# Performance work log

Measured on AMD Instinct MI355X. Metric: run time of the kernel, lower is better.

The kernel has to match this reference:

```python
import jax, jax.numpy as jnp
import numpy as np

M = 16            # num_frequencies
DIM = 512         # dim_input
B = 32768         # flattened batch
H = M + 1         # raw complex table side
N = 2 * M + 1     # autocorrelated table side
NPAR = H * H      # (m+1)^2


def setup_inputs() -> dict:
    key = jax.random.key(0)
    k1, k2, k3 = jax.random.split(key, 3)
    inputs = jax.random.normal(k1, (B, DIM), dtype=jnp.float32)
    targets = jax.random.uniform(k2, (B, 2), dtype=jnp.float32)  # points in [0,1) subset of [-1,1]^2
    # nn.init.normal_(weight, 0.01) => mean=0.01, std=1.0 ; bias zeros
    W = jax.random.normal(k3, (2 * NPAR, DIM), dtype=jnp.float32) + 0.01
    b = jnp.zeros((2 * NPAR,), dtype=jnp.float32)
    return {"inputs": inputs, "targets": targets, "W": W, "b": b}


def reference(inputs, targets, W, b):
    # Linear -> unconstrained complex (m+1)x(m+1) table per sample
    p = inputs @ W.T + b                                   # (B, 2*NPAR)
    real = p[:, :NPAR].reshape(-1, H, H)
    imag = p[:, NPAR:].reshape(-1, H, H)
    seq = jax.lax.complex(real, imag)                      # (B, H, H) complex64

    # 2D linear autocorrelation r[tau] = sum_i seq[i+tau] * conj(seq[i]),
    # tau in [-M, M]^2, via zero-padded FFT (equivalent to the grouped conv2d).
    F = jnp.fft.fft2(seq, s=(N, N))                        # (B, N, N)
    ac = jnp.fft.ifft2(F * jnp.conj(F))                    # circular autocorr
    ac = jnp.roll(ac, (M, M), axis=(-2, -1))               # index a -> lag a-M

    # Normalize so C[0,0] (= centre) equals 1/4 => unit mass on [-1,1]^2
    centre = ac[:, M, M].real                              # sum |seq|^2 > 0
    C = ac / (4.0 * centre)[:, None, None]                 # (B, N, N)

    # Evaluate f(x,y) = sum_{kx,ky} C * exp(i*pi*(kx*x + ky*y))
    k = jnp.arange(-M, M + 1, dtype=jnp.float32)
    kx, ky = jnp.meshgrid(k, k, indexing='xy')             # (N, N)
    tx = targets[:, 0][:, None, None]
    ty = targets[:, 1][:, None, None]
    phase = kx[None] * tx + ky[None] * ty                  # (B, N, N)
    exps = jnp.exp(1j * jnp.pi * phase)
    pdf = jnp.einsum('bij,bij->b', C, exps).real           # (B,)
    return pdf
```

## Files before the change

### kernel.cpp

```cpp
#include <hip/hip_runtime.h>

#define NPARC 289
#define NOUT  578
#define DIMK  512
#define CTILES 40
#define BATCH 32768
#define SPB   32

typedef __bf16 bf16x8 __attribute__((ext_vector_type(8)));
typedef float floatx4 __attribute__((ext_vector_type(4)));

__device__ __forceinline__ unsigned short f2bf(float f) {
    unsigned u = __float_as_uint(f);
    u = (u + 0x7fffu + ((u >> 16) & 1u)) >> 16;
    return (unsigned short)u;
}

__global__ void prep_w(const float* __restrict__ W, unsigned short* __restrict__ Wp) {
    int wid = threadIdx.x >> 6;
    int lane = threadIdx.x & 63;
    int col = blockIdx.x * 4 + wid;
    int k = lane * 8;
    unsigned short v[8];
    if (col < NOUT) {
        const float* src = W + (size_t)col * DIMK + k;
        #pragma unroll
        for (int j = 0; j < 8; ++j) v[j] = f2bf(src[j]);
    } else {
        #pragma unroll
        for (int j = 0; j < 8; ++j) v[j] = 0;
    }
    int ct = col >> 4;
    int ks = k >> 5;
    int ln = (((k >> 3) & 3) << 4) + (col & 15);
    uint4 o;
    o.x = (unsigned)v[0] | ((unsigned)v[1] << 16);
    o.y = (unsigned)v[2] | ((unsigned)v[3] << 16);
    o.z = (unsigned)v[4] | ((unsigned)v[5] << 16);
    o.w = (unsigned)v[6] | ((unsigned)v[7] << 16);
    *(uint4*)(Wp + (size_t)((ct * 16 + ks) * 64 + ln) * 8) = o;
}

__global__ __launch_bounds__(256, 4) void fused_kernel(
    const float* __restrict__ inputs, const float* __restrict__ targets,
    const float* __restrict__ bias, const unsigned short* __restrict__ Wp,
    float* __restrict__ out)
{
    __shared__ __align__(16) unsigned short Alds[SPB * 64 * 8];
    const int tid = threadIdx.x;
    const int base = blockIdx.x * SPB;

    const float4* inp4 = (const float4*)(inputs + (size_t)base * DIMK);
    #pragma unroll
    for (int i = 0; i < 16; ++i) {
        int f = i * 256 + tid;
        int s = f >> 7;
        int k = (f & 127) * 4;
        float4 v = inp4[f];
        int t = ((s >> 4) << 4) + (k >> 5);
        int ln = ((((k >> 3) & 3) << 4) + (s & 15)) ^ (t & 7);
        int off = (t * 64 + ln) * 8 + (k & 7);
        uint2 w;
        w.x = (unsigned)f2bf(v.x) | ((unsigned)f2bf(v.y) << 16);
        w.y = (unsigned)f2bf(v.z) | ((unsigned)f2bf(v.w) << 16);
        *(uint2*)&Alds[off] = w;
    }
    __syncthreads();

    const int wid  = tid >> 6;
    const int lane = tid & 63;
    const int quad = lane >> 4;
    const int lcol = lane & 15;

    float xs[2], ys[2];
    #pragma unroll
    for (int st = 0; st < 2; ++st) {
        float2 t2 = *(const float2*)(targets + 2 * (base + st * 16 + lcol));
        xs[st] = t2.x;
        ys[st] = t2.y;
    }

    float pd[2] = {0.f,0.f};
    float pr[2] = {0.f,0.f};
    float pim[2] = {0.f,0.f};

    const bf16x8* Wf = (const bf16x8*)Wp;

    #pragma unroll 1
    for (int pp = 0; pp < 5; ++pp) {
        const int wct0 = wid * 10 + pp * 2;
        floatx4 acc[2][2];
        #pragma unroll
        for (int w2 = 0; w2 < 2; ++w2)
            #pragma unroll
            for (int st = 0; st < 2; ++st) acc[w2][st] = (floatx4){0.f,0.f,0.f,0.f};

        #pragma unroll 4
        for (int ks = 0; ks < 16; ++ks) {
            bf16x8 aw[2], bs[2];
            #pragma unroll
            for (int w2 = 0; w2 < 2; ++w2)
                aw[w2] = Wf[(size_t)(((wct0 + w2) * 16 + ks) * 64 + lane)];
            const int lanex = lane ^ (ks & 7);
            #pragma unroll
            for (int st = 0; st < 2; ++st)
                bs[st] = *(const bf16x8*)&Alds[((st * 16 + ks) * 64 + lanex) * 8];
            #pragma unroll
            for (int w2 = 0; w2 < 2; ++w2)
                #pragma unroll
                for (int st = 0; st < 2; ++st)
                    acc[w2][st] = __builtin_amdgcn_mfma_f32_16x16x32_bf16(
                        aw[w2], bs[st], acc[w2][st], 0, 0, 0);
        }

        #pragma unroll
        for (int w2 = 0; w2 < 2; ++w2)
            #pragma unroll
            for (int reg = 0; reg < 4; ++reg) {
                int colw = (wct0 + w2) * 16 + quad * 4 + reg;
                if (colw < NOUT) {
                    bool im = (colw >= NPARC);
                    int idx = im ? colw - NPARC : colw;
                    int r = idx / 17;
                    int c = idx - r * 17;
                    float cf = (float)c, rf = (float)r;
                    float bb = bias[colw];
                    #pragma unroll
                    for (int st = 0; st < 2; ++st) {
                        float val = acc[w2][st][reg] + bb;
                        float phi = 3.14159265358979323846f * fmaf(cf, xs[st], rf * ys[st]);
                        float sn = __sinf(phi);
                        float cs = __cosf(phi);
                        float a1 = im ? -sn : cs;
                        float a2 = im ?  cs : sn;
                        pd[st]  = fmaf(val, val, pd[st]);
                        pr[st]  = fmaf(val, a1, pr[st]);
                        pim[st] = fmaf(val, a2, pim[st]);
                    }
                }
            }
    }

    #pragma unroll
    for (int d = 16; d < 64; d <<= 1)
        #pragma unroll
        for (int st = 0; st < 2; ++st) {
            pd[st]  += __shfl_xor(pd[st], d, 64);
            pr[st]  += __shfl_xor(pr[st], d, 64);
            pim[st] += __shfl_xor(pim[st], d, 64);
        }

    __syncthreads();
    float* R = (float*)Alds;
    if (lane < 16) {
        #pragma unroll
        for (int st = 0; st < 2; ++st) {
            int sl = st * 16 + lane;
            R[(wid * SPB + sl) * 3 + 0] = pd[st];
            R[(wid * SPB + sl) * 3 + 1] = pr[st];
            R[(wid * SPB + sl) * 3 + 2] = pim[st];
        }
    }
    __syncthreads();

    if (tid < SPB) {
        float sd = 0.f, sr = 0.f, si = 0.f;
        #pragma unroll
        for (int w = 0; w < 4; ++w) {
            sd += R[(w * SPB + tid) * 3 + 0];
            sr += R[(w * SPB + tid) * 3 + 1];
            si += R[(w * SPB + tid) * 3 + 2];
        }
        out[base + tid] = (sr * sr + si * si) / (4.0f * sd);
    }
}

extern "C" void kernel_launch(void* const* d_in, const int* in_sizes, int n_in,
                              void* d_out, int out_size, void* d_ws, size_t ws_size,
                              hipStream_t stream) {
    const float* inputs  = (const float*)d_in[0];
    const float* targets = (const float*)d_in[1];
    const float* W       = (const float*)d_in[2];
    const float* bias    = (const float*)d_in[3];
    unsigned short* Wp   = (unsigned short*)d_ws;

    prep_w<<<CTILES * 16 / 4, 256, 0, stream>>>(W, Wp);
    fused_kernel<<<BATCH / SPB, 256, 0, stream>>>(inputs, targets, bias, Wp, (float*)d_out);
}
```

Before: 126.0 us.

## Hold all ten column-tile accumulators and double-buffer W/A fragment loads across K

```diff
diff --git a/kernel.cpp b/kernel.cpp
--- a/kernel.cpp
+++ b/kernel.cpp
@@ -41,7 +41,7 @@
     *(uint4*)(Wp + (size_t)((ct * 16 + ks) * 64 + ln) * 8) = o;
 }
 
-__global__ __launch_bounds__(256, 4) void fused_kernel(
+__global__ __launch_bounds__(256, 3) void fused_kernel(
     const float* __restrict__ inputs, const float* __restrict__ targets,
     const float* __restrict__ bias, const unsigned short* __restrict__ Wp,
     float* __restrict__ out)
@@ -80,66 +80,80 @@
         ys[st] = t2.y;
     }
 
+    const bf16x8* Wf = (const bf16x8*)Wp;
+    const size_t awbase = (size_t)(wid * 10) * 16 * 64 + lane;
+
+    floatx4 acc[10][2];
+    #pragma unroll
+    for (int pp = 0; pp < 10; ++pp)
+        #pragma unroll
+        for (int st = 0; st < 2; ++st)
+            acc[pp][st] = (floatx4){0.f,0.f,0.f,0.f};
+
+    bf16x8 awA[10], awB[10], bsA[2], bsB[2];
+
+    auto loadAW = [&](bf16x8* dst, int ks) {
+        #pragma unroll
+        for (int pp = 0; pp < 10; ++pp)
+            dst[pp] = Wf[awbase + (size_t)(pp * 16 + ks) * 64];
+    };
+    auto loadBS = [&](bf16x8* dst, int ks) {
+        const int lanex = lane ^ (ks & 7);
+        #pragma unroll
+        for (int st = 0; st < 2; ++st)
+            dst[st] = *(const bf16x8*)&Alds[((st * 16 + ks) * 64 + lanex) * 8];
+    };
+    auto domfma = [&](const bf16x8* aw, const bf16x8* bs) {
+        #pragma unroll
+        for (int pp = 0; pp < 10; ++pp)
+            #pragma unroll
+            for (int st = 0; st < 2; ++st)
+                acc[pp][st] = __builtin_amdgcn_mfma_f32_16x16x32_bf16(
+                    aw[pp], bs[st], acc[pp][st], 0, 0, 0);
+    };
+
+    loadAW(awA, 0); loadBS(bsA, 0);
+    #pragma unroll 1
+    for (int k2 = 0; k2 < 7; ++k2) {
+        loadAW(awB, 2 * k2 + 1); loadBS(bsB, 2 * k2 + 1);
+        domfma(awA, bsA);
+        loadAW(awA, 2 * k2 + 2); loadBS(bsA, 2 * k2 + 2);
+        domfma(awB, bsB);
+    }
+    loadAW(awB, 15); loadBS(bsB, 15);
+    domfma(awA, bsA);
+    domfma(awB, bsB);
+
     float pd[2] = {0.f,0.f};
     float pr[2] = {0.f,0.f};
     float pim[2] = {0.f,0.f};
 
-    const bf16x8* Wf = (const bf16x8*)Wp;
-
-    #pragma unroll 1
-    for (int pp = 0; pp < 5; ++pp) {
-        const int wct0 = wid * 10 + pp * 2;
-        floatx4 acc[2][2];
-        #pragma unroll
-        for (int w2 = 0; w2 < 2; ++w2)
-            #pragma unroll
-            for (int st = 0; st < 2; ++st) acc[w2][st] = (floatx4){0.f,0.f,0.f,0.f};
-
-        #pragma unroll 4
-        for (int ks = 0; ks < 16; ++ks) {
-            bf16x8 aw[2], bs[2];
-            #pragma unroll
-            for (int w2 = 0; w2 < 2; ++w2)
-                aw[w2] = Wf[(size_t)(((wct0 + w2) * 16 + ks) * 64 + lane)];
-            const int lanex = lane ^ (ks & 7);
-            #pragma unroll
-            for (int st = 0; st < 2; ++st)
-                bs[st] = *(const bf16x8*)&Alds[((st * 16 + ks) * 64 + lanex) * 8];
-            #pragma unroll
-            for (int w2 = 0; w2 < 2; ++w2)
+    #pragma unroll
+    for (int pp = 0; pp < 10; ++pp)
+        #pragma unroll
+        for (int reg = 0; reg < 4; ++reg) {
+            int colw = (wid * 10 + pp) * 16 + quad * 4 + reg;
+            if (colw < NOUT) {
+                bool im = (colw >= NPARC);
+                int idx = im ? colw - NPARC : colw;
+                int r = idx / 17;
+                int c = idx - r * 17;
+                float cf = (float)c, rf = (float)r;
+                float bb = bias[colw];
                 #pragma unroll
-                for (int st = 0; st < 2; ++st)
-                    acc[w2][st] = __builtin_amdgcn_mfma_f32_16x16x32_bf16(
-                        aw[w2], bs[st], acc[w2][st], 0, 0, 0);
-        }
-
-        #pragma unroll
-        for (int w2 = 0; w2 < 2; ++w2)
-            #pragma unroll
-            for (int reg = 0; reg < 4; ++reg) {
-                int colw = (wct0 + w2) * 16 + quad * 4 + reg;
-                if (colw < NOUT) {
-                    bool im = (colw >= NPARC);
-                    int idx = im ? colw - NPARC : colw;
-                    int r = idx / 17;
-                    int c = idx - r * 17;
-                    float cf = (float)c, rf = (float)r;
-                    float bb = bias[colw];
-                    #pragma unroll
-                    for (int st = 0; st < 2; ++st) {
-                        float val = acc[w2][st][reg] + bb;
-                        float phi = 3.14159265358979323846f * fmaf(cf, xs[st], rf * ys[st]);
-                        float sn = __sinf(phi);
-                        float cs = __cosf(phi);
-                        float a1 = im ? -sn : cs;
-                        float a2 = im ?  cs : sn;
-                        pd[st]  = fmaf(val, val, pd[st]);
-                        pr[st]  = fmaf(val, a1, pr[st]);
-                        pim[st] = fmaf(val, a2, pim[st]);
-                    }
+                for (int st = 0; st < 2; ++st) {
+                    float val = acc[pp][st][reg] + bb;
+                    float phi = 3.14159265358979323846f * fmaf(cf, xs[st], rf * ys[st]);
+                    float sn = __sinf(phi);
+                    float cs = __cosf(phi);
+                    float a1 = im ? -sn : cs;
+                    float a2 = im ?  cs : sn;
+                    pd[st]  = fmaf(val, val, pd[st]);
+                    pr[st]  = fmaf(val, a1, pr[st]);
+                    pim[st] = fmaf(val, a2, pim[st]);
                 }
             }
-    }
+        }
 
     #pragma unroll
     for (int d = 16; d < 64; d <<= 1)
```

After: 139.3 us. 1.11x slower.

## Enlarge per-block tile to 64 samples with 5x4 MFMA register tile per wave

Applied to the files above, without the earlier changes.

```diff
diff --git a/kernel.cpp b/kernel.cpp
--- a/kernel.cpp
+++ b/kernel.cpp
@@ -5,7 +5,7 @@
 #define DIMK  512
 #define CTILES 40
 #define BATCH 32768
-#define SPB   32
+#define SPB   64
 
 typedef __bf16 bf16x8 __attribute__((ext_vector_type(8)));
 typedef float floatx4 __attribute__((ext_vector_type(4)));
@@ -41,7 +41,7 @@
     *(uint4*)(Wp + (size_t)((ct * 16 + ks) * 64 + ln) * 8) = o;
 }
 
-__global__ __launch_bounds__(256, 4) void fused_kernel(
+__global__ __launch_bounds__(256, 2) void fused_kernel(
     const float* __restrict__ inputs, const float* __restrict__ targets,
     const float* __restrict__ bias, const unsigned short* __restrict__ Wp,
     float* __restrict__ out)
@@ -52,7 +52,7 @@
 
     const float4* inp4 = (const float4*)(inputs + (size_t)base * DIMK);
     #pragma unroll
-    for (int i = 0; i < 16; ++i) {
+    for (int i = 0; i < 32; ++i) {
         int f = i * 256 + tid;
         int s = f >> 7;
         int k = (f & 127) * 4;
@@ -72,52 +72,54 @@
     const int quad = lane >> 4;
     const int lcol = lane & 15;
 
-    float xs[2], ys[2];
+    float xs[4], ys[4];
     #pragma unroll
-    for (int st = 0; st < 2; ++st) {
+    for (int st = 0; st < 4; ++st) {
         float2 t2 = *(const float2*)(targets + 2 * (base + st * 16 + lcol));
         xs[st] = t2.x;
         ys[st] = t2.y;
     }
 
-    float pd[2] = {0.f,0.f};
-    float pr[2] = {0.f,0.f};
-    float pim[2] = {0.f,0.f};
+    float pd[4]  = {0.f,0.f,0.f,0.f};
+    float pr[4]  = {0.f,0.f,0.f,0.f};
+    float pim[4] = {0.f,0.f,0.f,0.f};
 
     const bf16x8* Wf = (const bf16x8*)Wp;
 
     #pragma unroll 1
-    for (int pp = 0; pp < 5; ++pp) {
-        const int wct0 = wid * 10 + pp * 2;
-        floatx4 acc[2][2];
+    for (int p = 0; p < 2; ++p) {
+        const int wct0 = wid * 10 + p * 5;
+
+        floatx4 acc[5][4];
         #pragma unroll
-        for (int w2 = 0; w2 < 2; ++w2)
+        for (int pp = 0; pp < 5; ++pp)
             #pragma unroll
-            for (int st = 0; st < 2; ++st) acc[w2][st] = (floatx4){0.f,0.f,0.f,0.f};
+            for (int st = 0; st < 4; ++st)
+                acc[pp][st] = (floatx4){0.f,0.f,0.f,0.f};
 
-        #pragma unroll 4
+        #pragma unroll 2
         for (int ks = 0; ks < 16; ++ks) {
-            bf16x8 aw[2], bs[2];
+            const int lanex = lane ^ (ks & 7);
+            bf16x8 aw[5], bs[4];
             #pragma unroll
-            for (int w2 = 0; w2 < 2; ++w2)
-                aw[w2] = Wf[(size_t)(((wct0 + w2) * 16 + ks) * 64 + lane)];
-            const int lanex = lane ^ (ks & 7);
+            for (int pp = 0; pp < 5; ++pp)
+                aw[pp] = Wf[(size_t)(((wct0 + pp) * 16 + ks) * 64 + lane)];
             #pragma unroll
-            for (int st = 0; st < 2; ++st)
+            for (int st = 0; st < 4; ++st)
                 bs[st] = *(const bf16x8*)&Alds[((st * 16 + ks) * 64 + lanex) * 8];
             #pragma unroll
-            for (int w2 = 0; w2 < 2; ++w2)
+            for (int pp = 0; pp < 5; ++pp)
                 #pragma unroll
-                for (int st = 0; st < 2; ++st)
-                    acc[w2][st] = __builtin_amdgcn_mfma_f32_16x16x32_bf16(
-                        aw[w2], bs[st], acc[w2][st], 0, 0, 0);
+                for (int st = 0; st < 4; ++st)
+                    acc[pp][st] = __builtin_amdgcn_mfma_f32_16x16x32_bf16(
+                        aw[pp], bs[st], acc[pp][st], 0, 0, 0);
         }
 
         #pragma unroll
-        for (int w2 = 0; w2 < 2; ++w2)
+        for (int pp = 0; pp < 5; ++pp)
             #pragma unroll
             for (int reg = 0; reg < 4; ++reg) {
-                int colw = (wct0 + w2) * 16 + quad * 4 + reg;
+                int colw = (wct0 + pp) * 16 + quad * 4 + reg;
                 if (colw < NOUT) {
                     bool im = (colw >= NPARC);
                     int idx = im ? colw - NPARC : colw;
@@ -126,8 +128,8 @@
                     float cf = (float)c, rf = (float)r;
                     float bb = bias[colw];
                     #pragma unroll
-                    for (int st = 0; st < 2; ++st) {
-                        float val = acc[w2][st][reg] + bb;
+                    for (int st = 0; st < 4; ++st) {
+                        float val = acc[pp][st][reg] + bb;
                         float phi = 3.14159265358979323846f * fmaf(cf, xs[st], rf * ys[st]);
                         float sn = __sinf(phi);
                         float cs = __cosf(phi);
@@ -144,7 +146,7 @@
     #pragma unroll
     for (int d = 16; d < 64; d <<= 1)
         #pragma unroll
-        for (int st = 0; st < 2; ++st) {
+        for (int st = 0; st < 4; ++st) {
             pd[st]  += __shfl_xor(pd[st], d, 64);
             pr[st]  += __shfl_xor(pr[st], d, 64);
             pim[st] += __shfl_xor(pim[st], d, 64);
@@ -154,7 +156,7 @@
     float* R = (float*)Alds;
     if (lane < 16) {
         #pragma unroll
-        for (int st = 0; st < 2; ++st) {
+        for (int st = 0; st < 4; ++st) {
             int sl = st * 16 + lane;
             R[(wid * SPB + sl) * 3 + 0] = pd[st];
             R[(wid * SPB + sl) * 3 + 1] = pr[st];
```

After: 129.6 us. +2.9%, slower.
